# Kernel tuning notes

Hardware: AMD Instinct MI355X
Metric: run time of the kernel (lower is better)

The kernel has to match this reference:

```python
import jax, jax.numpy as jnp
import numpy as np

HEADS, DIM_HEAD, BITS = 12, 64, 4


def quantize(q, bits):
    # per-tensor affine fake-quant, exactly as the torch quantize()
    s = (q.max() - q.min()) / (2.0 ** bits - 1.0)
    z = jnp.round(2.0 ** bits - 1.0 - q.max() / s)
    return jnp.round(q / s + z), s, z


def setup_inputs() -> dict:
    key = jax.random.key(0)
    k1, k2, k3, k4 = jax.random.split(key, 4)
    return {
        "x": jax.random.normal(k1, (4, 1024, 768), jnp.float32),
        "w_qkv": jax.random.normal(k2, (2304, 768), jnp.float32) * 0.02,  # torch Linear weight [out,in]
        "w_out": jax.random.normal(k3, (768, 768), jnp.float32) * 0.02,
        "b_out": jax.random.normal(k4, (768,), jnp.float32) * 0.02,
    }


def reference(x, w_qkv, w_out, b_out):
    scale = DIM_HEAD ** -0.5
    B, N, D = x.shape
    # --- quantized QKV projection: x @ W^T with zero-point correction ---
    xq, sx1, zx1 = quantize(x, BITS)
    w1, sw1, zw1 = quantize(w_qkv.T, BITS)  # [D, 3*inner]
    xqkv = (xq @ w1
            - w1.sum(0, keepdims=True) * zx1
            - xq.sum(2, keepdims=True) * zw1
            + zx1 * zw1 * D) * (sx1 * sw1)  # [B, N, 3*inner]
    q, k, v = jnp.split(xqkv, 3, axis=-1)
    to_heads = lambda t: t.reshape(B, N, HEADS, DIM_HEAD).transpose(0, 2, 1, 3)  # b h n d
    q, k, v = to_heads(q), to_heads(k), to_heads(v)
    # --- quantized QK^T (note: original omits the +zq*zk*d term) ---
    qq, sq, zq = quantize(q, BITS)
    kq, sk, zk = quantize(k.transpose(0, 1, 3, 2), BITS)  # b h d n
    dots = (qq @ kq
            - kq.sum(2, keepdims=True) * zq
            - qq.sum(3, keepdims=True) * zk) * (scale * sq * sk)  # b h n n
    a = jax.nn.softmax(dots, axis=-1)
    # --- quantized A @ V ---
    aq, sa, za = quantize(a, BITS)
    vq, sv, zv = quantize(v, BITS)
    out = (aq @ vq
           - vq.sum(2, keepdims=True) * za
           - aq.sum(3, keepdims=True) * zv
           + za * zv * N) * (sa * sv)  # b h n d
    out = out.transpose(0, 2, 1, 3).reshape(B, N, HEADS * DIM_HEAD)
    # --- quantized output projection (faithful to original: correction uses
    # xqkv.sum / xqkv width, reproducing the source's use of `x` here) ---
    oq, sx2, zx2 = quantize(out, BITS)
    w2, sw2, zw2 = quantize(w_out.T, BITS)  # [inner, D]
    o = (oq @ w2
         - w2.sum(0, keepdims=True) * zx2
         - xqkv.sum(2, keepdims=True) * zw2
         + zx2 * zw2 * xqkv.shape[2]) * (sx2 * sw2) + b_out
    return o
```

## Files before the change

### kernel.cpp

```cpp
#include <hip/hip_runtime.h>
#include <math.h>

#define HEADS 12
#define DH    64
#define Dm    768
#define I3    2304
#define Nn    1024
#define Mm    4096
#define BHt   48
#define LOG2E 1.4426950408889634f

#define P_X  0
#define P_W1 1
#define P_Q  2
#define P_K  3
#define P_V  4
#define P_A  5
#define P_O  6
#define P_W2 7

typedef int v4i __attribute__((ext_vector_type(4)));

#if __has_builtin(__builtin_amdgcn_exp2f)
#define EXP2(x) __builtin_amdgcn_exp2f(x)
#else
#define EXP2(x) exp2f(x)
#endif

__device__ inline unsigned encf(float f) {
    unsigned u = __float_as_uint(f);
    return (u & 0x80000000u) ? ~u : (u | 0x80000000u);
}
__device__ inline float decf(unsigned u) {
    return (u & 0x80000000u) ? __uint_as_float(u & 0x7fffffffu) : __uint_as_float(~u);
}
__device__ inline void get_sz(const unsigned* scal, int pair, float* s, float* z) {
    float mn = decf(scal[2 * pair]);
    float mx = decf(scal[2 * pair + 1]);
    float ss = (mx - mn) / 15.0f;
    *s = ss;
    *z = rintf(15.0f - mx / ss);
}

__global__ __launch_bounds__(256) void k_init(unsigned* scal, float* z1, int n1, float* z2, int n2) {
    int g = blockIdx.x * 256 + threadIdx.x;
    if (g < n1) z1[g] = 0.f;
    if (g < n2) z2[g] = 0.f;
    if (g < 8) { scal[2 * g] = 0xFFFFFFFFu; scal[2 * g + 1] = 0u; }
}

__global__ __launch_bounds__(256) void k_minmax3(const float* x, const float* w1, const float* w2,
                                                 unsigned* scal) {
    __shared__ float rmn[256], rmx[256];
    int bid = blockIdx.x, tid = threadIdx.x;
    const float* src; int rows, pair, b0, nb;
    if (bid < 256)      { src = x;  rows = 4096; pair = P_X;  b0 = 0;   nb = 256; }
    else if (bid < 384) { src = w1; rows = 2304; pair = P_W1; b0 = 256; nb = 128; }
    else                { src = w2; rows = 768;  pair = P_W2; b0 = 384; nb = 64;  }
    float mn = INFINITY, mx = -INFINITY;
    for (int r = bid - b0; r < rows; r += nb) {
        const float* row = src + (long)r * 768;
#pragma unroll
        for (int k = 0; k < 3; ++k) {
            float v = row[tid + k * 256];
            mn = fminf(mn, v); mx = fmaxf(mx, v);
        }
    }
    rmn[tid] = mn; rmx[tid] = mx; __syncthreads();
    for (int s = 128; s > 0; s >>= 1) {
        if (tid < s) { rmn[tid] = fminf(rmn[tid], rmn[tid + s]); rmx[tid] = fmaxf(rmx[tid], rmx[tid + s]); }
        __syncthreads();
    }
    if (tid == 0) {
        atomicMin(&scal[2 * pair], encf(rmn[0]));
        atomicMax(&scal[2 * pair + 1], encf(rmx[0]));
    }
}

__global__ __launch_bounds__(256) void k_quant3(const float* x, const float* w1, const float* w2,
                                                const unsigned* scal,
                                                signed char* xq, signed char* wq, signed char* w2q,
                                                float* rs_x, float* rs_w1, float* rs_w2) {
    __shared__ float red[256];
    int bid = blockIdx.x, tid = threadIdx.x;
    const float* src; signed char* dq; float* rs; int pair, r;
    if (bid < 4096)      { src = x;  dq = xq;  rs = rs_x;  pair = P_X;  r = bid; }
    else if (bid < 6400) { src = w1; dq = wq;  rs = rs_w1; pair = P_W1; r = bid - 4096; }
    else                 { src = w2; dq = w2q; rs = rs_w2; pair = P_W2; r = bid - 6400; }
    float s, z; get_sz(scal, pair, &s, &z);
    const float* row = src + (long)r * 768;
    signed char* drow = dq + (long)r * 768;
    float acc = 0.f;
#pragma unroll
    for (int k = 0; k < 3; ++k) {
        int c = tid + k * 256;
        float q = rintf(row[c] / s + z);
        drow[c] = (signed char)(int)q;
        acc += q;
    }
    red[tid] = acc; __syncthreads();
    for (int s2 = 128; s2 > 0; s2 >>= 1) { if (tid < s2) red[tid] += red[tid + s2]; __syncthreads(); }
    if (tid == 0) rs[r] = red[0];
}

__global__ __launch_bounds__(256) void k_quant_rows(const float* src, const unsigned* scal, int pair,
                                                    signed char* dq, float* rowsum) {
    __shared__ float red[256];
    int r = blockIdx.x, tid = threadIdx.x;
    float s, z; get_sz(scal, pair, &s, &z);
    const float* row = src + (long)r * 768;
    signed char* drow = dq + (long)r * 768;
    float acc = 0.f;
#pragma unroll
    for (int k = 0; k < 3; ++k) {
        int c = tid + k * 256;
        float q = rintf(row[c] / s + z);
        drow[c] = (signed char)(int)q;
        acc += q;
    }
    red[tid] = acc; __syncthreads();
    for (int s2 = 128; s2 > 0; s2 >>= 1) { if (tid < s2) red[tid] += red[tid + s2]; __syncthreads(); }
    if (tid == 0) rowsum[r] = red[0];
}

__global__ __launch_bounds__(256) void k_gemm_mfma(const signed char* A, const signed char* B,
                                                   const float* colsumB, const float* rowsumA,
                                                   const float* bias, float* C, int K, int ldC,
                                                   const unsigned* scal, int pairA, int pairB,
                                                   float corrK, int do_stats, float* rowsum_out,
                                                   unsigned* scal_mm) {
    __shared__ __align__(16) signed char As[128 * 64];
    __shared__ __align__(16) signed char Bs[128 * 64];
    __shared__ float red[256];
    int tid = threadIdx.x;
    int wave = tid >> 6, lane = tid & 63;
    int col16 = lane & 15, quad = lane >> 4;
    long rowbase = (long)blockIdx.y * 128;
    long colbase = (long)blockIdx.x * 128;

    int c4 = tid & 3, r4 = tid >> 2;
    const signed char* ag0 = A + (rowbase + r4) * K + c4 * 16;
    const signed char* ag1 = A + (rowbase + r4 + 64) * K + c4 * 16;
    const signed char* bg0 = B + (colbase + r4) * K + c4 * 16;
    const signed char* bg1 = B + (colbase + r4 + 64) * K + c4 * 16;
    int soff0 = ((r4 >> 4) << 10) + (c4 << 8) + ((r4 & 15) << 4);
    int soff1 = soff0 + 4096;

    v4i ra0 = *(const v4i*)ag0;
    v4i ra1 = *(const v4i*)ag1;
    v4i rb0 = *(const v4i*)bg0;
    v4i rb1 = *(const v4i*)bg1;

    const int afrag_off = wave * 2048 + quad * 256 + col16 * 16;
    const int bfrag_off = quad * 256 + col16 * 16;
    v4i acc[2][8] = {};
    int nk = K >> 6;
    for (int kt = 0; kt < nk; ++kt) {
        *(v4i*)(As + soff0) = ra0;
        *(v4i*)(As + soff1) = ra1;
        *(v4i*)(Bs + soff0) = rb0;
        *(v4i*)(Bs + soff1) = rb1;
        __syncthreads();
        if (kt + 1 < nk) {
            int ko = (kt + 1) << 6;
            ra0 = *(const v4i*)(ag0 + ko);
            ra1 = *(const v4i*)(ag1 + ko);
            rb0 = *(const v4i*)(bg0 + ko);
            rb1 = *(const v4i*)(bg1 + ko);
        }
        v4i af0 = *(const v4i*)(As + afrag_off);
        v4i af1 = *(const v4i*)(As + afrag_off + 1024);
        v4i bf[8];
#pragma unroll
        for (int g = 0; g < 8; ++g) bf[g] = *(const v4i*)(Bs + bfrag_off + g * 1024);
#pragma unroll
        for (int g = 0; g < 8; ++g) {
            acc[0][g] = __builtin_amdgcn_mfma_i32_16x16x64_i8(af0, bf[g], acc[0][g], 0, 0, 0);
            acc[1][g] = __builtin_amdgcn_mfma_i32_16x16x64_i8(af1, bf[g], acc[1][g], 0, 0, 0);
        }
        __syncthreads();
    }

    float sA, zA, sB, zB;
    get_sz(scal, pairA, &sA, &zA);
    get_sz(scal, pairB, &sB, &zB);
    float sAB = sA * sB;
    float zz = (zA * zB) * corrK;
    float vmn = INFINITY, vmx = -INFINITY;
    float rowpart[2][4] = {};
#pragma unroll
    for (int i2 = 0; i2 < 2; ++i2)
#pragma unroll
        for (int g = 0; g < 8; ++g) {
            long col = colbase + g * 16 + col16;
            float cs = colsumB[col] * zA;
            float bv = bias ? bias[col] : 0.f;
#pragma unroll
            for (int r = 0; r < 4; ++r) {
                long row = rowbase + wave * 32 + i2 * 16 + quad * 4 + r;
                float v = ((float)acc[i2][g][r] - cs - rowsumA[row] * zB + zz) * sAB + bv;
                C[row * ldC + col] = v;
                rowpart[i2][r] += v;
                vmn = fminf(vmn, v); vmx = fmaxf(vmx, v);
            }
        }
    if (do_stats) {
#pragma unroll
        for (int i2 = 0; i2 < 2; ++i2)
#pragma unroll
            for (int r = 0; r < 4; ++r) {
                float s = rowpart[i2][r];
                s += __shfl_xor(s, 1); s += __shfl_xor(s, 2);
                s += __shfl_xor(s, 4); s += __shfl_xor(s, 8);
                if (col16 == 0)
                    atomicAdd(&rowsum_out[rowbase + wave * 32 + i2 * 16 + quad * 4 + r], s);
            }
        int pair = P_Q + (int)(colbase / 768);
        red[tid] = vmx; __syncthreads();
        for (int s = 128; s > 0; s >>= 1) { if (tid < s) red[tid] = fmaxf(red[tid], red[tid + s]); __syncthreads(); }
        if (tid == 0) atomicMax(&scal_mm[2 * pair + 1], encf(red[0]));
        __syncthreads();
        red[tid] = vmn; __syncthreads();
        for (int s = 128; s > 0; s >>= 1) { if (tid < s) red[tid] = fminf(red[tid], red[tid + s]); __syncthreads(); }
        if (tid == 0) atomicMin(&scal_mm[2 * pair], encf(red[0]));
    }
}

__global__ __launch_bounds__(256) void k_quant_qkv2(const float* xqkv, const unsigned* scal,
                                                    signed char* qq, signed char* kq, signed char* vqT,
                                                    float* rowsum_qq, float* cskc, float* colsum_vq) {
    __shared__ __align__(16) signed char vt[64 * 80];
    __shared__ float vred[4][64];
    int blk = blockIdx.x;
    int bh = blk >> 4, itile = blk & 15;
    int tid = threadIdx.x;
    int wave = tid >> 6, d = tid & 63;
    int b = bh / HEADS, h = bh - HEADS * b;
    float sq, zq, sk, zk, sv, zv;
    get_sz(scal, P_Q, &sq, &zq);
    get_sz(scal, P_K, &sk, &zk);
    get_sz(scal, P_V, &sv, &zv);
    float zqcsc2 = zq * ((0.125f * sq) * sk) * LOG2E;
    int vb = 0;
    float vsum = 0.f;
    for (int ir = 0; ir < 16; ++ir) {
        int il = wave * 16 + ir;
        int i = itile * 64 + il;
        const float* row = xqkv + ((long)b * Nn + i) * I3 + h * DH;
        float q = rintf(row[d] / sq + zq);
        float k = rintf(row[768 + d] / sk + zk);
        float v = rintf(row[1536 + d] / sv + zv);
        long o = ((long)bh * Nn + i) * 64 + d;
        qq[o] = (signed char)(int)q;
        kq[o] = (signed char)(int)k;
        vsum += v;
        vb |= ((int)v & 0xff) << ((ir & 3) * 8);
        if ((ir & 3) == 3) {
            *(int*)(vt + d * 80 + (il & ~3)) = vb;
            vb = 0;
        }
        float s1 = q, s2 = k;
        for (int off = 32; off > 0; off >>= 1) {
            s1 += __shfl_down(s1, off);
            s2 += __shfl_down(s2, off);
        }
        if (d == 0) { rowsum_qq[bh * Nn + i] = s1; cskc[bh * Nn + i] = s2 * zqcsc2; }
    }
    vred[wave][d] = vsum;
    __syncthreads();
    int dd = tid >> 2, c = tid & 3;
    *(v4i*)(vqT + ((long)bh * 64 + dd) * 1024 + itile * 64 + c * 16) = *(const v4i*)(vt + dd * 80 + c * 16);
    if (tid < 64)
        atomicAdd(&colsum_vq[bh * 64 + tid],
                  ((vred[0][tid] + vred[1][tid]) + vred[2][tid]) + vred[3][tid]);
}

__global__ __launch_bounds__(256) void k_attn_a6(const signed char* qq, const signed char* kq,
                                                 const float* rowsum_qq, const float* cskc,
                                                 unsigned* scal, float* rowmax, float* sumexp) {
    __shared__ float red[256];
    int blk = blockIdx.x;
    int bh = blk >> 4, itile = blk & 15;
    int tid = threadIdx.x;
    int wave = tid >> 6, lane = tid & 63;
    int col16 = lane & 15, quad = lane >> 4;
    int rowbase = itile * 64 + wave * 16;
    const signed char* kbase = kq + (long)bh * Nn * 64;
    const float* ck = cskc + bh * Nn;
    v4i afrag = *(const v4i*)(qq + ((long)bh * Nn + rowbase + col16) * 64 + quad * 16);
    float sq, zq, sk, zk;
    get_sz(scal, P_Q, &sq, &zq);
    get_sz(scal, P_K, &sk, &zk);
    float csc2 = ((0.125f * sq) * sk) * LOG2E;
    float rzc[4];
#pragma unroll
    for (int r = 0; r < 4; ++r)
        rzc[r] = rowsum_qq[bh * Nn + rowbase + quad * 4 + r] * zk * csc2;
    v4i zero = {0, 0, 0, 0};
    float m[4]    = {-INFINITY, -INFINITY, -INFINITY, -INFINITY};
    float se[4]   = {0.f, 0.f, 0.f, 0.f};
    float lmin[4] = {INFINITY, INFINITY, INFINITY, INFINITY};
    const signed char* kf = kbase + (long)col16 * 64 + quad * 16;
    v4i kb[2][4];
#pragma unroll
    for (int t = 0; t < 4; ++t) kb[0][t] = *(const v4i*)(kf + (long)(t * 16) * 64);
#pragma unroll 2
    for (int ch = 0; ch < 16; ++ch) {
        int cur = ch & 1, nxt = cur ^ 1;
        int pch = (ch < 15) ? ch + 1 : 15;
#pragma unroll
        for (int t = 0; t < 4; ++t)
            kb[nxt][t] = *(const v4i*)(kf + (long)(pch * 64 + t * 16) * 64);
#pragma unroll
        for (int t = 0; t < 4; ++t) {
            v4i d = __builtin_amdgcn_mfma_i32_16x16x64_i8(afrag, kb[cur][t], zero, 0, 0, 0);
            float ckv = ck[ch * 64 + t * 16 + col16];
#pragma unroll
            for (int r = 0; r < 4; ++r) {
                float dv = fmaf((float)d[r], csc2, -(ckv + rzc[r]));
                lmin[r] = fminf(lmin[r], dv);
                float mn = fmaxf(m[r], dv);
                se[r] = fmaf(se[r], EXP2(m[r] - mn), EXP2(dv - mn));
                m[r] = mn;
            }
        }
    }
#pragma unroll
    for (int r = 0; r < 4; ++r) {
#pragma unroll
        for (int off = 1; off < 16; off <<= 1) {
            float mo = __shfl_xor(m[r], off);
            float so = __shfl_xor(se[r], off);
            float mino = __shfl_xor(lmin[r], off);
            float mn = fmaxf(m[r], mo);
            se[r] = fmaf(se[r], EXP2(m[r] - mn), so * EXP2(mo - mn));
            m[r] = mn;
            lmin[r] = fminf(lmin[r], mino);
        }
    }
    float amax_c = -INFINITY, amin_c = INFINITY;
    if (col16 == 0) {
#pragma unroll
        for (int r = 0; r < 4; ++r) {
            int grow = bh * Nn + rowbase + quad * 4 + r;
            rowmax[grow] = m[r];
            sumexp[grow] = se[r];
            amax_c = fmaxf(amax_c, 1.0f / se[r]);
            amin_c = fminf(amin_c, EXP2(lmin[r] - m[r]) / se[r]);
        }
    }
    red[tid] = amax_c; __syncthreads();
    for (int s = 128; s > 0; s >>= 1) { if (tid < s) red[tid] = fmaxf(red[tid], red[tid + s]); __syncthreads(); }
    if (tid == 0) atomicMax(&scal[2 * P_A + 1], encf(red[0]));
    __syncthreads();
    red[tid] = amin_c; __syncthreads();
    for (int s = 128; s > 0; s >>= 1) { if (tid < s) red[tid] = fminf(red[tid], red[tid + s]); __syncthreads(); }
    if (tid == 0) atomicMin(&scal[2 * P_A], encf(red[0]));
}

__global__ __launch_bounds__(256) void k_attn_b6(const signed char* qq, const signed char* kq,
                                                 const signed char* vqT, const float* rowsum_qq,
                                                 const float* cskc, const float* colsum_vq,
                                                 const float* rowmax, const float* sumexp,
                                                 unsigned* scal, float* out_mat) {
    __shared__ __align__(16) signed char AqB[8192];
    __shared__ float red[256];
    int blk = blockIdx.x;
    int bh = blk >> 4, itile = blk & 15;
    int tid = threadIdx.x;
    int wave = tid >> 6, lane = tid & 63;
    int col16 = lane & 15, quad = lane >> 4;
    int rowbase = itile * 64 + wave * 16;
    int b = bh / HEADS, h = bh - HEADS * b;
    const signed char* kbase = kq + (long)bh * Nn * 64;
    const signed char* vbase = vqT + (long)bh * 64 * 1024;
    const float* ck = cskc + bh * Nn;
    v4i afrag = *(const v4i*)(qq + ((long)bh * Nn + rowbase + col16) * 64 + quad * 16);
    float sq, zq, sk, zk, sv, zv, sa, za;
    get_sz(scal, P_Q, &sq, &zq);
    get_sz(scal, P_K, &sk, &zk);
    get_sz(scal, P_V, &sv, &zv);
    get_sz(scal, P_A, &sa, &za);
    float csc2 = ((0.125f * sq) * sk) * LOG2E;
    float roff[4], crcp[4];
#pragma unroll
    for (int r = 0; r < 4; ++r) {
        int row = bh * Nn + rowbase + quad * 4 + r;
        roff[r] = rowsum_qq[row] * zk * csc2 + rowmax[row];
        crcp[r] = 1.0f / (sumexp[row] * sa);
    }
    v4i accPV[4] = {};
    v4i accOnes = {0, 0, 0, 0};
    v4i zero = {0, 0, 0, 0};
    v4i ones = {0x01010101, 0x01010101, 0x01010101, 0x01010101};
    for (int ch = 0; ch < 16; ++ch) {
        signed char* myAq = AqB + (ch & 1) * 4096 + wave * 1024;
#pragma unroll
        for (int t = 0; t < 4; ++t) {
            int jt = ch * 4 + t;
            v4i bfrag = *(const v4i*)(kbase + (long)(jt * 16 + col16) * 64 + quad * 16);
            v4i d = __builtin_amdgcn_mfma_i32_16x16x64_i8(afrag, bfrag, zero, 0, 0, 0);
            float ckv = ck[jt * 16 + col16];
#pragma unroll
            for (int r = 0; r < 4; ++r) {
                float es = fmaf((float)d[r], csc2, -(ckv + roff[r]));
                float fastv = fmaf(EXP2(es), crcp[r], za);
                float aqv = rintf(fastv);
                myAq[(quad * 4 + r) * 64 + t * 16 + col16] = (signed char)(int)aqv;
            }
        }
        asm volatile("s_waitcnt lgkmcnt(0)" ::: "memory");
        v4i pa = *(const v4i*)(myAq + col16 * 64 + quad * 16);
#pragma unroll
        for (int g = 0; g < 4; ++g) {
            v4i bv = *(const v4i*)(vbase + (long)(g * 16 + col16) * 1024 + ch * 64 + quad * 16);
            accPV[g] = __builtin_amdgcn_mfma_i32_16x16x64_i8(pa, bv, accPV[g], 0, 0, 0);
        }
        accOnes = __builtin_amdgcn_mfma_i32_16x16x64_i8(pa, ones, accOnes, 0, 0, 0);
    }
    float sav = sa * sv;
    float zz = (za * zv) * 1024.0f;
    float vmn = INFINITY, vmx = -INFINITY;
#pragma unroll
    for (int g = 0; g < 4; ++g) {
        int d = g * 16 + col16;
        float cs = colsum_vq[bh * 64 + d] * za;
#pragma unroll
        for (int r = 0; r < 4; ++r) {
            int i = rowbase + quad * 4 + r;
            float v = ((float)accPV[g][r] - cs - (float)accOnes[r] * zv + zz) * sav;
            out_mat[((long)b * Nn + i) * Dm + h * DH + d] = v;
            vmn = fminf(vmn, v); vmx = fmaxf(vmx, v);
        }
    }
    red[tid] = vmx; __syncthreads();
    for (int s = 128; s > 0; s >>= 1) { if (tid < s) red[tid] = fmaxf(red[tid], red[tid + s]); __syncthreads(); }
    if (tid == 0) atomicMax(&scal[2 * P_O + 1], encf(red[0]));
    __syncthreads();
    red[tid] = vmn; __syncthreads();
    for (int s = 128; s > 0; s >>= 1) { if (tid < s) red[tid] = fminf(red[tid], red[tid + s]); __syncthreads(); }
    if (tid == 0) atomicMin(&scal[2 * P_O], encf(red[0]));
}

extern "C" void kernel_launch(void* const* d_in, const int* in_sizes, int n_in,
                              void* d_out, int out_size, void* d_ws, size_t ws_size,
                              hipStream_t stream) {
    const float* x     = (const float*)d_in[0];
    const float* w_qkv = (const float*)d_in[1];
    const float* w_out = (const float*)d_in[2];
    const float* b_out = (const float*)d_in[3];

    char* ws = (char*)d_ws;
    size_t off = 0;
    auto alloc = [&](size_t n) -> char* {
        char* p = ws + off;
        off = (off + n + 255) & ~(size_t)255;
        return p;
    };
    unsigned*    scal        = (unsigned*)alloc(64);
    float*       xqkv        = (float*)alloc((size_t)Mm * I3 * 4);
    float*       out_mat     = (float*)alloc((size_t)Mm * Dm * 4);
    signed char* xq          = (signed char*)alloc((size_t)Mm * Dm);
    signed char* wq          = (signed char*)alloc((size_t)I3 * Dm);
    signed char* w2q         = (signed char*)alloc((size_t)Dm * Dm);
    signed char* oq          = (signed char*)alloc((size_t)Mm * Dm);
    signed char* qq          = (signed char*)alloc((size_t)BHt * Nn * DH);
    signed char* kq          = (signed char*)alloc((size_t)BHt * Nn * DH);
    signed char* vqT         = (signed char*)alloc((size_t)BHt * Nn * DH);
    float*       rowsum_xq   = (float*)alloc((size_t)Mm * 4);
    float*       colsum_w1   = (float*)alloc((size_t)I3 * 4);
    float*       colsum_w2   = (float*)alloc((size_t)Dm * 4);
    float*       rowsum_xqkv = (float*)alloc((size_t)Mm * 4);
    float*       rowsum_qq   = (float*)alloc((size_t)BHt * Nn * 4);
    float*       cskc        = (float*)alloc((size_t)BHt * Nn * 4);
    float*       colsum_vq   = (float*)alloc((size_t)BHt * DH * 4);
    float*       rowmax      = (float*)alloc((size_t)BHt * Nn * 4);
    float*       sumexp      = (float*)alloc((size_t)BHt * Nn * 4);
    float*       oq_rowsum   = (float*)alloc((size_t)Mm * 4);

    k_init<<<28, 256, 0, stream>>>(scal, rowsum_xqkv, Mm, colsum_vq, BHt * DH);

    k_minmax3<<<448, 256, 0, stream>>>(x, w_qkv, w_out, scal);
    k_quant3<<<7168, 256, 0, stream>>>(x, w_qkv, w_out, scal, xq, wq, w2q,
                                       rowsum_xq, colsum_w1, colsum_w2);

    {
        dim3 g(I3 / 128, Mm / 128);
        k_gemm_mfma<<<g, 256, 0, stream>>>(xq, wq, colsum_w1, rowsum_xq, nullptr, xqkv,
                                           Dm, I3, scal, P_X, P_W1, 768.0f,
                                           1, rowsum_xqkv, scal);
    }

    k_quant_qkv2<<<BHt * 16, 256, 0, stream>>>(xqkv, scal, qq, kq, vqT,
                                               rowsum_qq, cskc, colsum_vq);

    k_attn_a6<<<BHt * 16, 256, 0, stream>>>(qq, kq, rowsum_qq, cskc, scal, rowmax, sumexp);
    k_attn_b6<<<BHt * 16, 256, 0, stream>>>(qq, kq, vqT, rowsum_qq, cskc, colsum_vq,
                                            rowmax, sumexp, scal, out_mat);

    k_quant_rows<<<Mm, 256, 0, stream>>>(out_mat, scal, P_O, oq, oq_rowsum);

    {
        dim3 g(Dm / 128, Mm / 128);
        k_gemm_mfma<<<g, 256, 0, stream>>>(oq, w2q, colsum_w2, rowsum_xqkv, b_out, (float*)d_out,
                                           Dm, Dm, scal, P_O, P_W2, 2304.0f,
                                           0, nullptr, nullptr);
    }
}
```

Measured before the change: 263.8 us.

## Split attention key dimension across two wave groups per block

```diff
diff --git a/kernel.cpp b/kernel.cpp
--- a/kernel.cpp
+++ b/kernel.cpp
@@ -275,16 +275,18 @@
                   ((vred[0][tid] + vred[1][tid]) + vred[2][tid]) + vred[3][tid]);
 }
 
-__global__ __launch_bounds__(256) void k_attn_a6(const signed char* qq, const signed char* kq,
+__global__ __launch_bounds__(512) void k_attn_a7(const signed char* qq, const signed char* kq,
                                                  const float* rowsum_qq, const float* cskc,
                                                  unsigned* scal, float* rowmax, float* sumexp) {
-    __shared__ float red[256];
+    __shared__ float Wm[4][16], Wse[4][16], Wmin[4][16];
+    __shared__ float red[512];
     int blk = blockIdx.x;
     int bh = blk >> 4, itile = blk & 15;
     int tid = threadIdx.x;
     int wave = tid >> 6, lane = tid & 63;
     int col16 = lane & 15, quad = lane >> 4;
-    int rowbase = itile * 64 + wave * 16;
+    int wrg = wave & 3, kh = wave >> 2;
+    int rowbase = itile * 64 + wrg * 16;
     const signed char* kbase = kq + (long)bh * Nn * 64;
     const float* ck = cskc + bh * Nn;
     v4i afrag = *(const v4i*)(qq + ((long)bh * Nn + rowbase + col16) * 64 + quad * 16);
@@ -300,29 +302,18 @@
     float m[4]    = {-INFINITY, -INFINITY, -INFINITY, -INFINITY};
     float se[4]   = {0.f, 0.f, 0.f, 0.f};
     float lmin[4] = {INFINITY, INFINITY, INFINITY, INFINITY};
-    const signed char* kf = kbase + (long)col16 * 64 + quad * 16;
-    v4i kb[2][4];
-#pragma unroll
-    for (int t = 0; t < 4; ++t) kb[0][t] = *(const v4i*)(kf + (long)(t * 16) * 64);
-#pragma unroll 2
-    for (int ch = 0; ch < 16; ++ch) {
-        int cur = ch & 1, nxt = cur ^ 1;
-        int pch = (ch < 15) ? ch + 1 : 15;
-#pragma unroll
-        for (int t = 0; t < 4; ++t)
-            kb[nxt][t] = *(const v4i*)(kf + (long)(pch * 64 + t * 16) * 64);
-#pragma unroll
-        for (int t = 0; t < 4; ++t) {
-            v4i d = __builtin_amdgcn_mfma_i32_16x16x64_i8(afrag, kb[cur][t], zero, 0, 0, 0);
-            float ckv = ck[ch * 64 + t * 16 + col16];
-#pragma unroll
-            for (int r = 0; r < 4; ++r) {
-                float dv = fmaf((float)d[r], csc2, -(ckv + rzc[r]));
-                lmin[r] = fminf(lmin[r], dv);
-                float mn = fmaxf(m[r], dv);
-                se[r] = fmaf(se[r], EXP2(m[r] - mn), EXP2(dv - mn));
-                m[r] = mn;
-            }
+    for (int jt = 0; jt < 32; ++jt) {
+        int grp = kh * 32 + jt;
+        v4i bfrag = *(const v4i*)(kbase + (long)(grp * 16 + col16) * 64 + quad * 16);
+        v4i d = __builtin_amdgcn_mfma_i32_16x16x64_i8(afrag, bfrag, zero, 0, 0, 0);
+        float ckv = ck[grp * 16 + col16];
+#pragma unroll
+        for (int r = 0; r < 4; ++r) {
+            float dv = fmaf((float)d[r], csc2, -(ckv + rzc[r]));
+            lmin[r] = fminf(lmin[r], dv);
+            float mn = fmaxf(m[r], dv);
+            se[r] = fmaf(se[r], EXP2(m[r] - mn), EXP2(dv - mn));
+            m[r] = mn;
         }
     }
 #pragma unroll
@@ -338,39 +329,55 @@
             lmin[r] = fminf(lmin[r], mino);
         }
     }
+    if (kh == 1 && col16 == 0) {
+#pragma unroll
+        for (int r = 0; r < 4; ++r) {
+            Wm[wrg][quad * 4 + r] = m[r];
+            Wse[wrg][quad * 4 + r] = se[r];
+            Wmin[wrg][quad * 4 + r] = lmin[r];
+        }
+    }
+    __syncthreads();
     float amax_c = -INFINITY, amin_c = INFINITY;
-    if (col16 == 0) {
+    if (kh == 0 && col16 == 0) {
 #pragma unroll
         for (int r = 0; r < 4; ++r) {
-            int grow = bh * Nn + rowbase + quad * 4 + r;
-            rowmax[grow] = m[r];
-            sumexp[grow] = se[r];
-            amax_c = fmaxf(amax_c, 1.0f / se[r]);
-            amin_c = fminf(amin_c, EXP2(lmin[r] - m[r]) / se[r]);
+            int row = quad * 4 + r;
+            float mo = Wm[wrg][row], so = Wse[wrg][row], mino = Wmin[wrg][row];
+            float mn = fmaxf(m[r], mo);
+            float sef = fmaf(se[r], EXP2(m[r] - mn), so * EXP2(mo - mn));
+            float lmn = fminf(lmin[r], mino);
+            int grow = bh * Nn + rowbase + row;
+            rowmax[grow] = mn;
+            sumexp[grow] = sef;
+            amax_c = fmaxf(amax_c, 1.0f / sef);
+            amin_c = fminf(amin_c, EXP2(lmn - mn) / sef);
         }
     }
     red[tid] = amax_c; __syncthreads();
-    for (int s = 128; s > 0; s >>= 1) { if (tid < s) red[tid] = fmaxf(red[tid], red[tid + s]); __syncthreads(); }
+    for (int s = 256; s > 0; s >>= 1) { if (tid < s) red[tid] = fmaxf(red[tid], red[tid + s]); __syncthreads(); }
     if (tid == 0) atomicMax(&scal[2 * P_A + 1], encf(red[0]));
     __syncthreads();
     red[tid] = amin_c; __syncthreads();
-    for (int s = 128; s > 0; s >>= 1) { if (tid < s) red[tid] = fminf(red[tid], red[tid + s]); __syncthreads(); }
+    for (int s = 256; s > 0; s >>= 1) { if (tid < s) red[tid] = fminf(red[tid], red[tid + s]); __syncthreads(); }
     if (tid == 0) atomicMin(&scal[2 * P_A], encf(red[0]));
 }
 
-__global__ __launch_bounds__(256) void k_attn_b6(const signed char* qq, const signed char* kq,
+__global__ __launch_bounds__(512) void k_attn_b7(const signed char* qq, const signed char* kq,
                                                  const signed char* vqT, const float* rowsum_qq,
                                                  const float* cskc, const float* colsum_vq,
                                                  const float* rowmax, const float* sumexp,
                                                  unsigned* scal, float* out_mat) {
-    __shared__ __align__(16) signed char AqB[8192];
-    __shared__ float red[256];
+    __shared__ __align__(16) signed char AqB[16384];
+    __shared__ __align__(16) v4i onesX[4][64];
+    __shared__ float red[512];
     int blk = blockIdx.x;
     int bh = blk >> 4, itile = blk & 15;
     int tid = threadIdx.x;
     int wave = tid >> 6, lane = tid & 63;
     int col16 = lane & 15, quad = lane >> 4;
-    int rowbase = itile * 64 + wave * 16;
+    int wrg = wave & 3, kh = wave >> 2;
+    int rowbase = itile * 64 + wrg * 16;
     int b = bh / HEADS, h = bh - HEADS * b;
     const signed char* kbase = kq + (long)bh * Nn * 64;
     const signed char* vbase = vqT + (long)bh * 64 * 1024;
@@ -393,14 +400,14 @@
     v4i accOnes = {0, 0, 0, 0};
     v4i zero = {0, 0, 0, 0};
     v4i ones = {0x01010101, 0x01010101, 0x01010101, 0x01010101};
-    for (int ch = 0; ch < 16; ++ch) {
-        signed char* myAq = AqB + (ch & 1) * 4096 + wave * 1024;
+    for (int ch = 0; ch < 8; ++ch) {
+        signed char* myAq = AqB + (ch & 1) * 8192 + wave * 1024;
 #pragma unroll
         for (int t = 0; t < 4; ++t) {
-            int jt = ch * 4 + t;
-            v4i bfrag = *(const v4i*)(kbase + (long)(jt * 16 + col16) * 64 + quad * 16);
+            int grp = kh * 32 + ch * 4 + t;
+            v4i bfrag = *(const v4i*)(kbase + (long)(grp * 16 + col16) * 64 + quad * 16);
             v4i d = __builtin_amdgcn_mfma_i32_16x16x64_i8(afrag, bfrag, zero, 0, 0, 0);
-            float ckv = ck[jt * 16 + col16];
+            float ckv = ck[grp * 16 + col16];
 #pragma unroll
             for (int r = 0; r < 4; ++r) {
                 float es = fmaf((float)d[r], csc2, -(ckv + roff[r]));
@@ -413,32 +420,47 @@
         v4i pa = *(const v4i*)(myAq + col16 * 64 + quad * 16);
 #pragma unroll
         for (int g = 0; g < 4; ++g) {
-            v4i bv = *(const v4i*)(vbase + (long)(g * 16 + col16) * 1024 + ch * 64 + quad * 16);
+            v4i bv = *(const v4i*)(vbase + (long)(g * 16 + col16) * 1024 + kh * 512 + ch * 64 + quad * 16);
             accPV[g] = __builtin_amdgcn_mfma_i32_16x16x64_i8(pa, bv, accPV[g], 0, 0, 0);
         }
         accOnes = __builtin_amdgcn_mfma_i32_16x16x64_i8(pa, ones, accOnes, 0, 0, 0);
     }
-    float sav = sa * sv;
-    float zz = (za * zv) * 1024.0f;
+    __syncthreads();
+    if (kh == 1) {
+        v4i* ex = (v4i*)AqB;
+#pragma unroll
+        for (int g = 0; g < 4; ++g) ex[((wrg * 64) + lane) * 4 + g] = accPV[g];
+        onesX[wrg][lane] = accOnes;
+    }
+    __syncthreads();
     float vmn = INFINITY, vmx = -INFINITY;
-#pragma unroll
-    for (int g = 0; g < 4; ++g) {
-        int d = g * 16 + col16;
-        float cs = colsum_vq[bh * 64 + d] * za;
-#pragma unroll
-        for (int r = 0; r < 4; ++r) {
-            int i = rowbase + quad * 4 + r;
-            float v = ((float)accPV[g][r] - cs - (float)accOnes[r] * zv + zz) * sav;
-            out_mat[((long)b * Nn + i) * Dm + h * DH + d] = v;
-            vmn = fminf(vmn, v); vmx = fmaxf(vmx, v);
+    if (kh == 0) {
+        const v4i* ex = (const v4i*)AqB;
+        v4i po = onesX[wrg][lane];
+        accOnes = accOnes + po;
+        float sav = sa * sv;
+        float zz = (za * zv) * 1024.0f;
+#pragma unroll
+        for (int g = 0; g < 4; ++g) {
+            v4i pg = ex[((wrg * 64) + lane) * 4 + g];
+            accPV[g] = accPV[g] + pg;
+            int d = g * 16 + col16;
+            float cs = colsum_vq[bh * 64 + d] * za;
+#pragma unroll
+            for (int r = 0; r < 4; ++r) {
+                int i = rowbase + quad * 4 + r;
+                float v = ((float)accPV[g][r] - cs - (float)accOnes[r] * zv + zz) * sav;
+                out_mat[((long)b * Nn + i) * Dm + h * DH + d] = v;
+                vmn = fminf(vmn, v); vmx = fmaxf(vmx, v);
+            }
         }
     }
     red[tid] = vmx; __syncthreads();
-    for (int s = 128; s > 0; s >>= 1) { if (tid < s) red[tid] = fmaxf(red[tid], red[tid + s]); __syncthreads(); }
+    for (int s = 256; s > 0; s >>= 1) { if (tid < s) red[tid] = fmaxf(red[tid], red[tid + s]); __syncthreads(); }
     if (tid == 0) atomicMax(&scal[2 * P_O + 1], encf(red[0]));
     __syncthreads();
     red[tid] = vmn; __syncthreads();
-    for (int s = 128; s > 0; s >>= 1) { if (tid < s) red[tid] = fminf(red[tid], red[tid + s]); __syncthreads(); }
+    for (int s = 256; s > 0; s >>= 1) { if (tid < s) red[tid] = fminf(red[tid], red[tid + s]); __syncthreads(); }
     if (tid == 0) atomicMin(&scal[2 * P_O], encf(red[0]));
 }
 
@@ -494,8 +516,8 @@
     k_quant_qkv2<<<BHt * 16, 256, 0, stream>>>(xqkv, scal, qq, kq, vqT,
                                                rowsum_qq, cskc, colsum_vq);
 
-    k_attn_a6<<<BHt * 16, 256, 0, stream>>>(qq, kq, rowsum_qq, cskc, scal, rowmax, sumexp);
-    k_attn_b6<<<BHt * 16, 256, 0, stream>>>(qq, kq, vqT, rowsum_qq, cskc, colsum_vq,
+    k_attn_a7<<<BHt * 16, 512, 0, stream>>>(qq, kq, rowsum_qq, cskc, scal, rowmax, sumexp);
+    k_attn_b7<<<BHt * 16, 512, 0, stream>>>(qq, kq, vqT, rowsum_qq, cskc, colsum_vq,
                                             rowmax, sumexp, scal, out_mat);
 
     k_quant_rows<<<Mm, 256, 0, stream>>>(out_mat, scal, P_O, oq, oq_rowsum);
```

Result: slower. 269.2 us (+2.0%).

## Software-pipeline softmax quantization with PV MFMA and drop unused row sums

Applied to the files above, without the earlier changes.

```diff
diff --git a/kernel.cpp b/kernel.cpp
--- a/kernel.cpp
+++ b/kernel.cpp
@@ -104,23 +104,17 @@
 }
 
 __global__ __launch_bounds__(256) void k_quant_rows(const float* src, const unsigned* scal, int pair,
-                                                    signed char* dq, float* rowsum) {
-    __shared__ float red[256];
+                                                    signed char* dq) {
     int r = blockIdx.x, tid = threadIdx.x;
     float s, z; get_sz(scal, pair, &s, &z);
     const float* row = src + (long)r * 768;
     signed char* drow = dq + (long)r * 768;
-    float acc = 0.f;
 #pragma unroll
     for (int k = 0; k < 3; ++k) {
         int c = tid + k * 256;
         float q = rintf(row[c] / s + z);
         drow[c] = (signed char)(int)q;
-        acc += q;
-    }
-    red[tid] = acc; __syncthreads();
-    for (int s2 = 128; s2 > 0; s2 >>= 1) { if (tid < s2) red[tid] += red[tid + s2]; __syncthreads(); }
-    if (tid == 0) rowsum[r] = red[0];
+    }
 }
 
 __global__ __launch_bounds__(256) void k_gemm_mfma(const signed char* A, const signed char* B,
@@ -275,7 +269,7 @@
                   ((vred[0][tid] + vred[1][tid]) + vred[2][tid]) + vred[3][tid]);
 }
 
-__global__ __launch_bounds__(256) void k_attn_a6(const signed char* qq, const signed char* kq,
+__global__ __launch_bounds__(256) void k_attn_a8(const signed char* qq, const signed char* kq,
                                                  const float* rowsum_qq, const float* cskc,
                                                  unsigned* scal, float* rowmax, float* sumexp) {
     __shared__ float red[256];
@@ -358,7 +352,7 @@
     if (tid == 0) atomicMin(&scal[2 * P_A], encf(red[0]));
 }
 
-__global__ __launch_bounds__(256) void k_attn_b6(const signed char* qq, const signed char* kq,
+__global__ __launch_bounds__(256) void k_attn_b8(const signed char* qq, const signed char* kq,
                                                  const signed char* vqT, const float* rowsum_qq,
                                                  const float* cskc, const float* colsum_vq,
                                                  const float* rowmax, const float* sumexp,
@@ -390,34 +384,47 @@
         crcp[r] = 1.0f / (sumexp[row] * sa);
     }
     v4i accPV[4] = {};
-    v4i accOnes = {0, 0, 0, 0};
+    float rs_a[4] = {0.f, 0.f, 0.f, 0.f};
     v4i zero = {0, 0, 0, 0};
-    v4i ones = {0x01010101, 0x01010101, 0x01010101, 0x01010101};
+
+#define QUANT_CHUNK(CH, BUF)                                                            \
+    {                                                                                   \
+        signed char* myAq = AqB + (BUF) * 4096 + wave * 1024;                           \
+        _Pragma("unroll")                                                               \
+        for (int t = 0; t < 4; ++t) {                                                   \
+            int jt = (CH) * 4 + t;                                                      \
+            v4i bfrag = *(const v4i*)(kbase + (long)(jt * 16 + col16) * 64 + quad * 16);\
+            v4i d = __builtin_amdgcn_mfma_i32_16x16x64_i8(afrag, bfrag, zero, 0, 0, 0); \
+            float ckv = ck[jt * 16 + col16];                                            \
+            _Pragma("unroll")                                                           \
+            for (int r = 0; r < 4; ++r) {                                               \
+                float es = fmaf((float)d[r], csc2, -(ckv + roff[r]));                   \
+                float fastv = fmaf(EXP2(es), crcp[r], za);                              \
+                float aqv = rintf(fastv);                                               \
+                rs_a[r] += aqv;                                                         \
+                myAq[(quad * 4 + r) * 64 + t * 16 + col16] = (signed char)(int)aqv;     \
+            }                                                                           \
+        }                                                                               \
+    }
+
+    QUANT_CHUNK(0, 0)
     for (int ch = 0; ch < 16; ++ch) {
-        signed char* myAq = AqB + (ch & 1) * 4096 + wave * 1024;
-#pragma unroll
-        for (int t = 0; t < 4; ++t) {
-            int jt = ch * 4 + t;
-            v4i bfrag = *(const v4i*)(kbase + (long)(jt * 16 + col16) * 64 + quad * 16);
-            v4i d = __builtin_amdgcn_mfma_i32_16x16x64_i8(afrag, bfrag, zero, 0, 0, 0);
-            float ckv = ck[jt * 16 + col16];
-#pragma unroll
-            for (int r = 0; r < 4; ++r) {
-                float es = fmaf((float)d[r], csc2, -(ckv + roff[r]));
-                float fastv = fmaf(EXP2(es), crcp[r], za);
-                float aqv = rintf(fastv);
-                myAq[(quad * 4 + r) * 64 + t * 16 + col16] = (signed char)(int)aqv;
-            }
-        }
-        asm volatile("s_waitcnt lgkmcnt(0)" ::: "memory");
-        v4i pa = *(const v4i*)(myAq + col16 * 64 + quad * 16);
-#pragma unroll
-        for (int g = 0; g < 4; ++g) {
-            v4i bv = *(const v4i*)(vbase + (long)(g * 16 + col16) * 1024 + ch * 64 + quad * 16);
-            accPV[g] = __builtin_amdgcn_mfma_i32_16x16x64_i8(pa, bv, accPV[g], 0, 0, 0);
-        }
-        accOnes = __builtin_amdgcn_mfma_i32_16x16x64_i8(pa, ones, accOnes, 0, 0, 0);
-    }
+        int cur = ch & 1;
+        v4i pa = *(const v4i*)(AqB + cur * 4096 + wave * 1024 + col16 * 64 + quad * 16);
+        v4i bv[4];
+#pragma unroll
+        for (int g = 0; g < 4; ++g)
+            bv[g] = *(const v4i*)(vbase + (long)(g * 16 + col16) * 1024 + ch * 64 + quad * 16);
+        if (ch < 15) QUANT_CHUNK(ch + 1, cur ^ 1)
+#pragma unroll
+        for (int g = 0; g < 4; ++g)
+            accPV[g] = __builtin_amdgcn_mfma_i32_16x16x64_i8(pa, bv[g], accPV[g], 0, 0, 0);
+    }
+#undef QUANT_CHUNK
+
+#pragma unroll
+    for (int r = 0; r < 4; ++r)
+        for (int off = 1; off < 16; off <<= 1) rs_a[r] += __shfl_xor(rs_a[r], off);
     float sav = sa * sv;
     float zz = (za * zv) * 1024.0f;
     float vmn = INFINITY, vmx = -INFINITY;
@@ -428,7 +435,7 @@
 #pragma unroll
         for (int r = 0; r < 4; ++r) {
             int i = rowbase + quad * 4 + r;
-            float v = ((float)accPV[g][r] - cs - (float)accOnes[r] * zv + zz) * sav;
+            float v = ((float)accPV[g][r] - cs - rs_a[r] * zv + zz) * sav;
             out_mat[((long)b * Nn + i) * Dm + h * DH + d] = v;
             vmn = fminf(vmn, v); vmx = fmaxf(vmx, v);
         }
@@ -476,7 +483,6 @@
     float*       colsum_vq   = (float*)alloc((size_t)BHt * DH * 4);
     float*       rowmax      = (float*)alloc((size_t)BHt * Nn * 4);
     float*       sumexp      = (float*)alloc((size_t)BHt * Nn * 4);
-    float*       oq_rowsum   = (float*)alloc((size_t)Mm * 4);
 
     k_init<<<28, 256, 0, stream>>>(scal, rowsum_xqkv, Mm, colsum_vq, BHt * DH);
 
@@ -494,11 +500,11 @@
     k_quant_qkv2<<<BHt * 16, 256, 0, stream>>>(xqkv, scal, qq, kq, vqT,
                                                rowsum_qq, cskc, colsum_vq);
 
-    k_attn_a6<<<BHt * 16, 256, 0, stream>>>(qq, kq, rowsum_qq, cskc, scal, rowmax, sumexp);
-    k_attn_b6<<<BHt * 16, 256, 0, stream>>>(qq, kq, vqT, rowsum_qq, cskc, colsum_vq,
+    k_attn_a8<<<BHt * 16, 256, 0, stream>>>(qq, kq, rowsum_qq, cskc, scal, rowmax, sumexp);
+    k_attn_b8<<<BHt * 16, 256, 0, stream>>>(qq, kq, vqT, rowsum_qq, cskc, colsum_vq,
                                             rowmax, sumexp, scal, out_mat);
 
-    k_quant_rows<<<Mm, 256, 0, stream>>>(out_mat, scal, P_O, oq, oq_rowsum);
+    k_quant_rows<<<Mm, 256, 0, stream>>>(out_mat, scal, P_O, oq);
 
     {
         dim3 g(Dm / 128, Mm / 128);
```

Measured after the change: 259.4 us. Within noise of the previous version (-1.7%).
